# Kernel tuning notes

Measured on AMD Instinct MI355X. Metric: run time of the kernel, lower is better.

The kernel has to match this reference:

```python
import jax, jax.numpy as jnp
import numpy as np

N_NODES = 100000
N_EDGES = 800000
NUM_FEATURES = 64
HIDDEN = 16
N_GRAPHS = 64


def setup_inputs() -> dict:
    key = jax.random.key(0)
    ks = jax.random.split(key, 12)
    x = jax.random.normal(ks[0], (N_NODES, NUM_FEATURES), dtype=jnp.float32)
    edge_index = jax.random.randint(ks[1], (2, N_EDGES), 0, N_NODES, dtype=jnp.int64)
    batch = jnp.sort(jax.random.randint(ks[2], (N_NODES,), 0, N_GRAPHS, dtype=jnp.int64))
    def glorot(k, shape):
        fan_in, fan_out = shape
        s = jnp.sqrt(2.0 / (fan_in + fan_out))
        return jax.random.normal(k, shape, dtype=jnp.float32) * s
    return {
        "x": x,
        "edge_index": edge_index,
        "batch": batch,
        "W1_rel": glorot(ks[3], (NUM_FEATURES, HIDDEN)),
        "W1_root": glorot(ks[4], (NUM_FEATURES, HIDDEN)),
        "b1": jnp.zeros((HIDDEN,), dtype=jnp.float32),
        "W2_rel": glorot(ks[5], (HIDDEN, HIDDEN)),
        "W2_root": glorot(ks[6], (HIDDEN, HIDDEN)),
        "b2": jnp.zeros((HIDDEN,), dtype=jnp.float32),
        "Wlin": glorot(ks[7], (HIDDEN, 1)),
        "blin": jnp.zeros((1,), dtype=jnp.float32),
    }


def _graph_conv(h, src, dst, W_rel, W_root, b):
    # PyG GraphConv: out_i = W_rel @ sum_{j->i} h_j + b + W_root @ h_i
    agg = jax.ops.segment_sum(h[src], dst, num_segments=h.shape[0])
    return agg @ W_rel + b + h @ W_root


def reference(x, edge_index, batch, W1_rel, W1_root, b1, W2_rel, W2_root, b2, Wlin, blin):
    src, dst = edge_index[0], edge_index[1]
    h = jax.nn.relu(_graph_conv(x, src, dst, W1_rel, W1_root, b1))
    # F.dropout(training=False) is identity at inference
    h = _graph_conv(h, src, dst, W2_rel, W2_root, b2)
    # global mean pool over graphs
    sums = jax.ops.segment_sum(h, batch, num_segments=N_GRAPHS)  # [G, H]
    counts = jax.ops.segment_sum(jnp.ones((h.shape[0],), dtype=h.dtype), batch, num_segments=N_GRAPHS)
    pooled = sums / jnp.maximum(counts, 1.0)[:, None]
    out = pooled @ Wlin + blin  # [G, 1]
    return out.squeeze(1)
```

## Files before the change

### kernel.cpp

```cpp
#include <hip/hip_runtime.h>
#include <hip/hip_fp16.h>

#define BUCKET_BITS 7
#define BUCKET_N    128
#define SEG_CAP     1280
#define EPB         4096
#define EPT         16
#define OVF_CAP     16384
#define MAXBUCK     1024

__global__ __launch_bounds__(256) void k_phase1(
    const float* __restrict__ x, const float* __restrict__ Wrel,
    const float* __restrict__ Wroot, const float* __restrict__ bias,
    const int* __restrict__ src, const int* __restrict__ dst,
    __half* __restrict__ p1, float* __restrict__ r1,
    int* __restrict__ cursor, int2* __restrict__ seg,
    int* __restrict__ ovf_n, int2* __restrict__ ovf,
    int n_nodes, int n_edges, int nbuck, int tb)
{
    __shared__ int smem[2080];
    const int t = threadIdx.x;

    if ((int)blockIdx.x < tb) {
        float* s_wr = (float*)smem;
        float* s_wo = (float*)(smem + 1024);
        float* s_b  = (float*)(smem + 2048);
        for (int i = t; i < 1024; i += 256) { s_wr[i] = Wrel[i]; s_wo[i] = Wroot[i]; }
        if (t < 16) s_b[t] = bias[t];
        __syncthreads();

        const int node = blockIdx.x * 256 + t;
        if (node >= n_nodes) return;

        float accr[16], acco[16];
#pragma unroll
        for (int o = 0; o < 16; ++o) { accr[o] = 0.f; acco[o] = 0.f; }

        const float* xr = x + (size_t)node * 64;
        for (int c = 0; c < 4; ++c) {
            float4 xv[4];
#pragma unroll
            for (int u = 0; u < 4; ++u) xv[u] = *(const float4*)(xr + c * 16 + u * 4);
#pragma unroll
            for (int u = 0; u < 4; ++u) {
                const float xs[4] = {xv[u].x, xv[u].y, xv[u].z, xv[u].w};
#pragma unroll
                for (int kk = 0; kk < 4; ++kk) {
                    const int k = c * 16 + u * 4 + kk;
                    const float xk = xs[kk];
                    const float4* wr4 = (const float4*)&s_wr[k * 16];
                    const float4* wo4 = (const float4*)&s_wo[k * 16];
#pragma unroll
                    for (int q = 0; q < 4; ++q) {
                        const float4 wr = wr4[q], wo = wo4[q];
                        accr[q * 4 + 0] = fmaf(xk, wr.x, accr[q * 4 + 0]);
                        accr[q * 4 + 1] = fmaf(xk, wr.y, accr[q * 4 + 1]);
                        accr[q * 4 + 2] = fmaf(xk, wr.z, accr[q * 4 + 2]);
                        accr[q * 4 + 3] = fmaf(xk, wr.w, accr[q * 4 + 3]);
                        acco[q * 4 + 0] = fmaf(xk, wo.x, acco[q * 4 + 0]);
                        acco[q * 4 + 1] = fmaf(xk, wo.y, acco[q * 4 + 1]);
                        acco[q * 4 + 2] = fmaf(xk, wo.z, acco[q * 4 + 2]);
                        acco[q * 4 + 3] = fmaf(xk, wo.w, acco[q * 4 + 3]);
                    }
                }
            }
        }

        __half2 ph[8];
#pragma unroll
        for (int k = 0; k < 8; ++k)
            ph[k] = __floats2half2_rn(accr[2 * k], accr[2 * k + 1]);
        ((uint4*)(p1 + (size_t)node * 16))[0] = ((const uint4*)ph)[0];
        ((uint4*)(p1 + (size_t)node * 16))[1] = ((const uint4*)ph)[1];
        float* rr = r1 + (size_t)node * 16;
#pragma unroll
        for (int q = 0; q < 4; ++q) {
            float4 v;
            v.x = acco[q * 4 + 0] + s_b[q * 4 + 0];
            v.y = acco[q * 4 + 1] + s_b[q * 4 + 1];
            v.z = acco[q * 4 + 2] + s_b[q * 4 + 2];
            v.w = acco[q * 4 + 3] + s_b[q * 4 + 3];
            *(float4*)(rr + q * 4) = v;
        }
    } else {
        int* hist = smem;
        int* base = smem + 1024;
        for (int i = t; i < nbuck; i += 256) hist[i] = 0;
        __syncthreads();

        const int e0 = ((int)blockIdx.x - tb) * EPB;
        int es[EPT], ed[EPT], ep[EPT];
#pragma unroll
        for (int k = 0; k < EPT; ++k) {
            const int e = e0 + k * 256 + t;
            if (e < n_edges) {
                ed[k] = dst[e];
                es[k] = src[e];
                ep[k] = atomicAdd(&hist[ed[k] >> BUCKET_BITS], 1);
            } else ed[k] = -1;
        }
        __syncthreads();
        for (int b = t; b < nbuck; b += 256) {
            const int h = hist[b];
            base[b] = h ? atomicAdd(&cursor[b * 16], h) : 0;
        }
        __syncthreads();
#pragma unroll
        for (int k = 0; k < EPT; ++k) {
            if (ed[k] >= 0) {
                const int b = ed[k] >> BUCKET_BITS;
                const int rel = base[b] + ep[k];
                if (rel < SEG_CAP) {
                    seg[b * SEG_CAP + rel] = make_int2(es[k], ed[k]);
                } else {
                    const int op = atomicAdd(ovf_n, 1);
                    if (op < OVF_CAP) ovf[op] = make_int2(es[k], ed[k]);
                }
            }
        }
    }
}

__device__ inline void acc_half8(float* acc, uint4 raw) {
    const __half2* h2 = (const __half2*)&raw;
#pragma unroll
    for (int k = 0; k < 4; ++k) {
        const float2 f = __half22float2(h2[k]);
        acc[2 * k]     += f.x;
        acc[2 * k + 1] += f.y;
    }
}

__global__ __launch_bounds__(256) void k_aggregate(
    const __half* __restrict__ p1, const float* __restrict__ r1,
    const int2* __restrict__ seg, const int* __restrict__ cursor,
    const int* __restrict__ ovf_n, const int2* __restrict__ ovf,
    const int* __restrict__ batch,
    const float* __restrict__ W2rel, const float* __restrict__ W2root,
    const float* __restrict__ Wlin,
    float* __restrict__ s_out, float* __restrict__ T2, float* __restrict__ cntg,
    int* __restrict__ g_sorted, int* __restrict__ g_beg, int* __restrict__ g_cnt,
    int n_nodes)
{
    __shared__ int s_src[SEG_CAP];
    __shared__ int hist[BUCKET_N];
    __shared__ int iscan[BUCKET_N];
    __shared__ int cur[BUCKET_N];
    __shared__ float s_w2r[16], s_w2o[16];
    __shared__ float sT2[64], scnt[64];
    __shared__ int s_no, s_w0;

    const int t = threadIdx.x, b = blockIdx.x;
    if (t < BUCKET_N) hist[t] = 0;
    if (t < 16) {
        float ar = 0.f, ao = 0.f;
#pragma unroll
        for (int o = 0; o < 16; ++o) {
            const float wl = Wlin[o];
            ar = fmaf(W2rel[t * 16 + o], wl, ar);
            ao = fmaf(W2root[t * 16 + o], wl, ao);
        }
        s_w2r[t] = ar; s_w2o[t] = ao;
    }
    if (t < 64) { sT2[t] = 0.f; scnt[t] = 0.f; }
    if (t == 0) s_no = min(*ovf_n, OVF_CAP);
    __syncthreads();

    const int bstart = b * SEG_CAP;
    const int count = min(cursor[b * 16], SEG_CAP);

    int2 er[5];
    int ne = 0;
    for (int i = t; i < count; i += 256) {
        er[ne] = seg[bstart + i];
        atomicAdd(&hist[er[ne].y & (BUCKET_N - 1)], 1);
        ++ne;
    }
    __syncthreads();
    int v = 0;
    if (t < BUCKET_N) {
        v = hist[t];
#pragma unroll
        for (int off = 1; off < 64; off <<= 1) {
            const int u = __shfl_up(v, off);
            if ((t & 63) >= off) v += u;
        }
        if (t == 63) s_w0 = v;
    }
    __syncthreads();
    if (t < BUCKET_N) {
        if (t >= 64) v += s_w0;
        iscan[t] = v;
        cur[t] = v - hist[t];
    }
    __syncthreads();
    for (int k = 0; k < ne; ++k)
        s_src[atomicAdd(&cur[er[k].y & (BUCKET_N - 1)], 1)] = er[k].x;
    __syncthreads();

    for (int i = t; i < count; i += 256) g_sorted[bstart + i] = s_src[i];
    if (t < BUCKET_N) {
        const int nodew = b * BUCKET_N + t;
        if (nodew < n_nodes) {
            g_beg[nodew] = bstart + iscan[t] - hist[t];
            g_cnt[nodew] = hist[t];
        }
    }

    const int nl = t >> 1, half = t & 1;
    const int node = b * BUCKET_N + nl;
    if (node < n_nodes) {
        const int end = iscan[nl];
        const int beg = end - hist[nl];
        float acc[8] = {0.f, 0.f, 0.f, 0.f, 0.f, 0.f, 0.f, 0.f};
        int j = beg;
        for (; j + 2 <= end; j += 2) {
            const int s0 = s_src[j], s1 = s_src[j + 1];
            const uint4 a = *(const uint4*)(p1 + (size_t)s0 * 16 + half * 8);
            const uint4 c = *(const uint4*)(p1 + (size_t)s1 * 16 + half * 8);
            acc_half8(acc, a);
            acc_half8(acc, c);
        }
        if (j < end) {
            const uint4 a = *(const uint4*)(p1 + (size_t)s_src[j] * 16 + half * 8);
            acc_half8(acc, a);
        }
        for (int ov = 0; ov < s_no; ++ov) {
            const int2 e = ovf[ov];
            if (e.y == node) {
                const uint4 a = *(const uint4*)(p1 + (size_t)e.x * 16 + half * 8);
                acc_half8(acc, a);
            }
        }
        const float4 rA = *(const float4*)(r1 + (size_t)node * 16 + half * 8);
        const float4 rB = *(const float4*)(r1 + (size_t)node * 16 + half * 8 + 4);
        float h[8];
        h[0] = fmaxf(acc[0] + rA.x, 0.f); h[1] = fmaxf(acc[1] + rA.y, 0.f);
        h[2] = fmaxf(acc[2] + rA.z, 0.f); h[3] = fmaxf(acc[3] + rA.w, 0.f);
        h[4] = fmaxf(acc[4] + rB.x, 0.f); h[5] = fmaxf(acc[5] + rB.y, 0.f);
        h[6] = fmaxf(acc[6] + rB.z, 0.f); h[7] = fmaxf(acc[7] + rB.w, 0.f);
        float ps = 0.f, pu = 0.f;
#pragma unroll
        for (int k = 0; k < 8; ++k) {
            ps = fmaf(h[k], s_w2r[half * 8 + k], ps);
            pu = fmaf(h[k], s_w2o[half * 8 + k], pu);
        }
        ps += __shfl_xor(ps, 1);
        pu += __shfl_xor(pu, 1);
        if (half == 0) {
            s_out[node] = ps;
            const int g = batch[node];
            atomicAdd(&sT2[g], pu);
            atomicAdd(&scnt[g], 1.f);
        }
    }
    __syncthreads();
    if (t < 64) {
        if (sT2[t] != 0.f) unsafeAtomicAdd(&T2[t], sT2[t]);
        if (scnt[t] != 0.f) unsafeAtomicAdd(&cntg[t], scnt[t]);
    }
}

__global__ __launch_bounds__(256) void k_T1(
    const float* __restrict__ s_in, const int* __restrict__ g_sorted,
    const int* __restrict__ g_beg, const int* __restrict__ g_cnt,
    const int* __restrict__ batch,
    const int* __restrict__ ovf_n, const int2* __restrict__ ovf,
    float* __restrict__ T1, int n_nodes)
{
    __shared__ float bins[64];
    const int t = threadIdx.x;
    if (t < 64) bins[t] = 0.f;
    __syncthreads();

    const int node = blockIdx.x * 256 + t;
    if (node < n_nodes) {
        const int beg = g_beg[node], c = g_cnt[node];
        float acc = 0.f;
        int j = 0;
        for (; j + 4 <= c; j += 4) {
            const int a = g_sorted[beg + j],      b2 = g_sorted[beg + j + 1];
            const int cc = g_sorted[beg + j + 2], d = g_sorted[beg + j + 3];
            acc += s_in[a] + s_in[b2] + s_in[cc] + s_in[d];
        }
        for (; j < c; ++j) acc += s_in[g_sorted[beg + j]];
        if (acc != 0.f) atomicAdd(&bins[batch[node]], acc);
    }
    __syncthreads();
    if (t < 64 && bins[t] != 0.f) unsafeAtomicAdd(&T1[t], bins[t]);

    if (blockIdx.x == 0) {
        const int n = min(*ovf_n, OVF_CAP);
        for (int i = t; i < n; i += 256)
            unsafeAtomicAdd(&T1[batch[ovf[i].y]], s_in[ovf[i].x]);
    }
}

__global__ void k_finalize(
    const float* __restrict__ T1, const float* __restrict__ T2,
    const float* __restrict__ cntg, const float* __restrict__ b2,
    const float* __restrict__ Wlin, const float* __restrict__ blin,
    float* __restrict__ out, int n_graphs)
{
    const int g = threadIdx.x;
    if (g >= n_graphs) return;
    float cb = 0.f;
#pragma unroll
    for (int o = 0; o < 16; ++o) cb = fmaf(b2[o], Wlin[o], cb);
    const float c = fmaxf(cntg[g], 1.f);
    out[g] = (T1[g] + T2[g]) / c + cb + blin[0];
}

extern "C" void kernel_launch(void* const* d_in, const int* in_sizes, int n_in,
                              void* d_out, int out_size, void* d_ws, size_t ws_size,
                              hipStream_t stream) {
    const float* x       = (const float*)d_in[0];
    const int*   ei      = (const int*)d_in[1];
    const int*   batch   = (const int*)d_in[2];
    const float* W1_rel  = (const float*)d_in[3];
    const float* W1_root = (const float*)d_in[4];
    const float* b1      = (const float*)d_in[5];
    const float* W2_rel  = (const float*)d_in[6];
    const float* W2_root = (const float*)d_in[7];
    const float* b2      = (const float*)d_in[8];
    const float* Wlin    = (const float*)d_in[9];
    const float* blin    = (const float*)d_in[10];
    float* out = (float*)d_out;

    const int N = in_sizes[0] / 64;
    const int E = in_sizes[1] / 2;
    const int G = out_size;
    const int nbuck = (N + BUCKET_N - 1) >> BUCKET_BITS;

    const int* src = ei;
    const int* dst = ei + E;

    auto rnd4 = [](size_t v) { return (v + 3) & ~(size_t)3; };
    float* ws = (float*)d_ws;
    size_t off = 0;
    __half* p1      = (__half*)(ws + off); off += rnd4((size_t)N * 8);
    float* r1       = ws + off; off += rnd4((size_t)N * 16);
    float* s_buf    = ws + off; off += rnd4((size_t)N);
    int*   cursor   = (int*)(ws + off); off += rnd4((size_t)nbuck * 16);
    int*   ovf_n    = (int*)(ws + off); off += 4;
    float* T1       = ws + off; off += rnd4((size_t)G);
    float* T2       = ws + off; off += rnd4((size_t)G);
    float* cntg     = ws + off; off += rnd4((size_t)G);
    int2*  seg      = (int2*)(ws + off); off += rnd4((size_t)nbuck * SEG_CAP * 2);
    int*   g_sorted = (int*)(ws + off); off += rnd4((size_t)nbuck * SEG_CAP);
    int*   g_beg    = (int*)(ws + off); off += rnd4((size_t)N);
    int*   g_cnt    = (int*)(ws + off); off += rnd4((size_t)N);
    int2*  ovf      = (int2*)(ws + off); off += rnd4((size_t)OVF_CAP * 2);

    hipMemsetAsync(cursor, 0, ((size_t)nbuck * 16 + 4 + 3 * rnd4((size_t)G)) * sizeof(int), stream);

    const int tb = (N + 255) / 256;
    const int sb = (E + EPB - 1) / EPB;
    const int ab = (N + 255) / 256;

    k_phase1   <<<tb + sb, 256, 0, stream>>>(x, W1_rel, W1_root, b1, src, dst,
                                             p1, r1, cursor, seg, ovf_n, ovf,
                                             N, E, nbuck, tb);
    k_aggregate<<<nbuck, 256, 0, stream>>>(p1, r1, seg, cursor, ovf_n, ovf, batch,
                                           W2_rel, W2_root, Wlin, s_buf, T2, cntg,
                                           g_sorted, g_beg, g_cnt, N);
    k_T1       <<<ab, 256, 0, stream>>>(s_buf, g_sorted, g_beg, g_cnt, batch,
                                        ovf_n, ovf, T1, N);
    k_finalize <<<1, 64, 0, stream>>>(T1, T2, cntg, b2, Wlin, blin, out, G);
}
```

Baseline: 158.8 us.

## Fuse all stages into one persistent cooperative kernel with grid syncs

Replaces the four separate launches with a single cooperative persistent kernel (512 blocks, falling back to 256 or to the old multi-kernel path) that loops over work units and uses grid.sync between the transform/bin, aggregate, T1 and finalize stages. It also packs each binned edge into one int (src shifted left by 7, dst low bits) instead of an int2, halving segment-buffer traffic. The aim is to remove kernel launch gaps and inter-kernel drain. In exchange, grid-wide barriers cost time, the fixed grid may underuse the GPU for some phases, and the packing assumes node indices fit in 24 bits.

```diff
diff --git a/kernel.cpp b/kernel.cpp
--- a/kernel.cpp
+++ b/kernel.cpp
@@ -1,5 +1,8 @@
 #include <hip/hip_runtime.h>
 #include <hip/hip_fp16.h>
+#include <hip/hip_cooperative_groups.h>
+
+namespace cg = cooperative_groups;
 
 #define BUCKET_BITS 7
 #define BUCKET_N    128
@@ -7,119 +10,6 @@
 #define EPB         4096
 #define EPT         16
 #define OVF_CAP     16384
-#define MAXBUCK     1024
-
-__global__ __launch_bounds__(256) void k_phase1(
-    const float* __restrict__ x, const float* __restrict__ Wrel,
-    const float* __restrict__ Wroot, const float* __restrict__ bias,
-    const int* __restrict__ src, const int* __restrict__ dst,
-    __half* __restrict__ p1, float* __restrict__ r1,
-    int* __restrict__ cursor, int2* __restrict__ seg,
-    int* __restrict__ ovf_n, int2* __restrict__ ovf,
-    int n_nodes, int n_edges, int nbuck, int tb)
-{
-    __shared__ int smem[2080];
-    const int t = threadIdx.x;
-
-    if ((int)blockIdx.x < tb) {
-        float* s_wr = (float*)smem;
-        float* s_wo = (float*)(smem + 1024);
-        float* s_b  = (float*)(smem + 2048);
-        for (int i = t; i < 1024; i += 256) { s_wr[i] = Wrel[i]; s_wo[i] = Wroot[i]; }
-        if (t < 16) s_b[t] = bias[t];
-        __syncthreads();
-
-        const int node = blockIdx.x * 256 + t;
-        if (node >= n_nodes) return;
-
-        float accr[16], acco[16];
-#pragma unroll
-        for (int o = 0; o < 16; ++o) { accr[o] = 0.f; acco[o] = 0.f; }
-
-        const float* xr = x + (size_t)node * 64;
-        for (int c = 0; c < 4; ++c) {
-            float4 xv[4];
-#pragma unroll
-            for (int u = 0; u < 4; ++u) xv[u] = *(const float4*)(xr + c * 16 + u * 4);
-#pragma unroll
-            for (int u = 0; u < 4; ++u) {
-                const float xs[4] = {xv[u].x, xv[u].y, xv[u].z, xv[u].w};
-#pragma unroll
-                for (int kk = 0; kk < 4; ++kk) {
-                    const int k = c * 16 + u * 4 + kk;
-                    const float xk = xs[kk];
-                    const float4* wr4 = (const float4*)&s_wr[k * 16];
-                    const float4* wo4 = (const float4*)&s_wo[k * 16];
-#pragma unroll
-                    for (int q = 0; q < 4; ++q) {
-                        const float4 wr = wr4[q], wo = wo4[q];
-                        accr[q * 4 + 0] = fmaf(xk, wr.x, accr[q * 4 + 0]);
-                        accr[q * 4 + 1] = fmaf(xk, wr.y, accr[q * 4 + 1]);
-                        accr[q * 4 + 2] = fmaf(xk, wr.z, accr[q * 4 + 2]);
-                        accr[q * 4 + 3] = fmaf(xk, wr.w, accr[q * 4 + 3]);
-                        acco[q * 4 + 0] = fmaf(xk, wo.x, acco[q * 4 + 0]);
-                        acco[q * 4 + 1] = fmaf(xk, wo.y, acco[q * 4 + 1]);
-                        acco[q * 4 + 2] = fmaf(xk, wo.z, acco[q * 4 + 2]);
-                        acco[q * 4 + 3] = fmaf(xk, wo.w, acco[q * 4 + 3]);
-                    }
-                }
-            }
-        }
-
-        __half2 ph[8];
-#pragma unroll
-        for (int k = 0; k < 8; ++k)
-            ph[k] = __floats2half2_rn(accr[2 * k], accr[2 * k + 1]);
-        ((uint4*)(p1 + (size_t)node * 16))[0] = ((const uint4*)ph)[0];
-        ((uint4*)(p1 + (size_t)node * 16))[1] = ((const uint4*)ph)[1];
-        float* rr = r1 + (size_t)node * 16;
-#pragma unroll
-        for (int q = 0; q < 4; ++q) {
-            float4 v;
-            v.x = acco[q * 4 + 0] + s_b[q * 4 + 0];
-            v.y = acco[q * 4 + 1] + s_b[q * 4 + 1];
-            v.z = acco[q * 4 + 2] + s_b[q * 4 + 2];
-            v.w = acco[q * 4 + 3] + s_b[q * 4 + 3];
-            *(float4*)(rr + q * 4) = v;
-        }
-    } else {
-        int* hist = smem;
-        int* base = smem + 1024;
-        for (int i = t; i < nbuck; i += 256) hist[i] = 0;
-        __syncthreads();
-
-        const int e0 = ((int)blockIdx.x - tb) * EPB;
-        int es[EPT], ed[EPT], ep[EPT];
-#pragma unroll
-        for (int k = 0; k < EPT; ++k) {
-            const int e = e0 + k * 256 + t;
-            if (e < n_edges) {
-                ed[k] = dst[e];
-                es[k] = src[e];
-                ep[k] = atomicAdd(&hist[ed[k] >> BUCKET_BITS], 1);
-            } else ed[k] = -1;
-        }
-        __syncthreads();
-        for (int b = t; b < nbuck; b += 256) {
-            const int h = hist[b];
-            base[b] = h ? atomicAdd(&cursor[b * 16], h) : 0;
-        }
-        __syncthreads();
-#pragma unroll
-        for (int k = 0; k < EPT; ++k) {
-            if (ed[k] >= 0) {
-                const int b = ed[k] >> BUCKET_BITS;
-                const int rel = base[b] + ep[k];
-                if (rel < SEG_CAP) {
-                    seg[b * SEG_CAP + rel] = make_int2(es[k], ed[k]);
-                } else {
-                    const int op = atomicAdd(ovf_n, 1);
-                    if (op < OVF_CAP) ovf[op] = make_int2(es[k], ed[k]);
-                }
-            }
-        }
-    }
-}
 
 __device__ inline void acc_half8(float* acc, uint4 raw) {
     const __half2* h2 = (const __half2*)&raw;
@@ -131,26 +21,118 @@
     }
 }
 
-__global__ __launch_bounds__(256) void k_aggregate(
+
+__device__ __forceinline__ void transform_unit(
+    int unit, int t, int N,
+    const float* __restrict__ x, float* s_wr, float* s_wo, float* s_b,
+    __half* __restrict__ p1, float* __restrict__ r1)
+{
+    const int node = unit * 256 + t;
+    if (node >= N) return;
+    float accr[16], acco[16];
+#pragma unroll
+    for (int o = 0; o < 16; ++o) { accr[o] = 0.f; acco[o] = 0.f; }
+    const float* xr = x + (size_t)node * 64;
+    for (int c = 0; c < 4; ++c) {
+        float4 xv[4];
+#pragma unroll
+        for (int u = 0; u < 4; ++u) xv[u] = *(const float4*)(xr + c * 16 + u * 4);
+#pragma unroll
+        for (int u = 0; u < 4; ++u) {
+            const float xs[4] = {xv[u].x, xv[u].y, xv[u].z, xv[u].w};
+#pragma unroll
+            for (int kk = 0; kk < 4; ++kk) {
+                const int k = c * 16 + u * 4 + kk;
+                const float xk = xs[kk];
+                const float4* wr4 = (const float4*)&s_wr[k * 16];
+                const float4* wo4 = (const float4*)&s_wo[k * 16];
+#pragma unroll
+                for (int q = 0; q < 4; ++q) {
+                    const float4 wr = wr4[q], wo = wo4[q];
+                    accr[q * 4 + 0] = fmaf(xk, wr.x, accr[q * 4 + 0]);
+                    accr[q * 4 + 1] = fmaf(xk, wr.y, accr[q * 4 + 1]);
+                    accr[q * 4 + 2] = fmaf(xk, wr.z, accr[q * 4 + 2]);
+                    accr[q * 4 + 3] = fmaf(xk, wr.w, accr[q * 4 + 3]);
+                    acco[q * 4 + 0] = fmaf(xk, wo.x, acco[q * 4 + 0]);
+                    acco[q * 4 + 1] = fmaf(xk, wo.y, acco[q * 4 + 1]);
+                    acco[q * 4 + 2] = fmaf(xk, wo.z, acco[q * 4 + 2]);
+                    acco[q * 4 + 3] = fmaf(xk, wo.w, acco[q * 4 + 3]);
+                }
+            }
+        }
+    }
+    __half2 ph[8];
+#pragma unroll
+    for (int k = 0; k < 8; ++k)
+        ph[k] = __floats2half2_rn(accr[2 * k], accr[2 * k + 1]);
+    ((uint4*)(p1 + (size_t)node * 16))[0] = ((const uint4*)ph)[0];
+    ((uint4*)(p1 + (size_t)node * 16))[1] = ((const uint4*)ph)[1];
+    float* rr = r1 + (size_t)node * 16;
+#pragma unroll
+    for (int q = 0; q < 4; ++q) {
+        float4 v;
+        v.x = acco[q * 4 + 0] + s_b[q * 4 + 0];
+        v.y = acco[q * 4 + 1] + s_b[q * 4 + 1];
+        v.z = acco[q * 4 + 2] + s_b[q * 4 + 2];
+        v.w = acco[q * 4 + 3] + s_b[q * 4 + 3];
+        *(float4*)(rr + q * 4) = v;
+    }
+}
+
+__device__ __forceinline__ void bin_unit(
+    int unit, int t, int E, int nbuck,
+    const int* __restrict__ src, const int* __restrict__ dst,
+    int* hist, int* base,
+    int* __restrict__ cursor, int* __restrict__ seg,
+    int* __restrict__ ovf_n, int2* __restrict__ ovf)
+{
+    for (int i = t; i < nbuck; i += 256) hist[i] = 0;
+    __syncthreads();
+    const int e0 = unit * EPB;
+    int es[EPT], ed[EPT], ep[EPT];
+#pragma unroll
+    for (int k = 0; k < EPT; ++k) {
+        const int e = e0 + k * 256 + t;
+        if (e < E) {
+            ed[k] = dst[e];
+            es[k] = src[e];
+            ep[k] = atomicAdd(&hist[ed[k] >> BUCKET_BITS], 1);
+        } else ed[k] = -1;
+    }
+    __syncthreads();
+    for (int b = t; b < nbuck; b += 256) {
+        const int h = hist[b];
+        base[b] = h ? atomicAdd(&cursor[b * 16], h) : 0;
+    }
+    __syncthreads();
+#pragma unroll
+    for (int k = 0; k < EPT; ++k) {
+        if (ed[k] >= 0) {
+            const int b = ed[k] >> BUCKET_BITS;
+            const int rel = base[b] + ep[k];
+            if (rel < SEG_CAP) {
+                seg[b * SEG_CAP + rel] = (es[k] << BUCKET_BITS) | (ed[k] & (BUCKET_N - 1));
+            } else {
+                const int op = atomicAdd(ovf_n, 1);
+                if (op < OVF_CAP) ovf[op] = make_int2(es[k], ed[k]);
+            }
+        }
+    }
+}
+
+__device__ __forceinline__ void aggregate_unit(
+    int b, int t, int N,
     const __half* __restrict__ p1, const float* __restrict__ r1,
-    const int2* __restrict__ seg, const int* __restrict__ cursor,
+    const int* __restrict__ seg, const int* __restrict__ cursor,
     const int* __restrict__ ovf_n, const int2* __restrict__ ovf,
     const int* __restrict__ batch,
     const float* __restrict__ W2rel, const float* __restrict__ W2root,
     const float* __restrict__ Wlin,
-    float* __restrict__ s_out, float* __restrict__ T2, float* __restrict__ cntg,
+    float* __restrict__ s_out, float* __restrict__ T2g, float* __restrict__ cntg,
     int* __restrict__ g_sorted, int* __restrict__ g_beg, int* __restrict__ g_cnt,
-    int n_nodes)
-{
-    __shared__ int s_src[SEG_CAP];
-    __shared__ int hist[BUCKET_N];
-    __shared__ int iscan[BUCKET_N];
-    __shared__ int cur[BUCKET_N];
-    __shared__ float s_w2r[16], s_w2o[16];
-    __shared__ float sT2[64], scnt[64];
-    __shared__ int s_no, s_w0;
-
-    const int t = threadIdx.x, b = blockIdx.x;
+    int* s_src, int* hist, int* iscan, int* cur,
+    float* w2r, float* w2o, float* sT2, float* scnt, int* s_no, int* s_w0)
+{
     if (t < BUCKET_N) hist[t] = 0;
     if (t < 16) {
         float ar = 0.f, ao = 0.f;
@@ -160,20 +142,20 @@
             ar = fmaf(W2rel[t * 16 + o], wl, ar);
             ao = fmaf(W2root[t * 16 + o], wl, ao);
         }
-        s_w2r[t] = ar; s_w2o[t] = ao;
+        w2r[t] = ar; w2o[t] = ao;
     }
     if (t < 64) { sT2[t] = 0.f; scnt[t] = 0.f; }
-    if (t == 0) s_no = min(*ovf_n, OVF_CAP);
+    if (t == 0) *s_no = min(*ovf_n, OVF_CAP);
     __syncthreads();
 
     const int bstart = b * SEG_CAP;
     const int count = min(cursor[b * 16], SEG_CAP);
 
-    int2 er[5];
+    int er[5];
     int ne = 0;
     for (int i = t; i < count; i += 256) {
         er[ne] = seg[bstart + i];
-        atomicAdd(&hist[er[ne].y & (BUCKET_N - 1)], 1);
+        atomicAdd(&hist[er[ne] & (BUCKET_N - 1)], 1);
         ++ne;
     }
     __syncthreads();
@@ -185,23 +167,23 @@
             const int u = __shfl_up(v, off);
             if ((t & 63) >= off) v += u;
         }
-        if (t == 63) s_w0 = v;
+        if (t == 63) *s_w0 = v;
     }
     __syncthreads();
     if (t < BUCKET_N) {
-        if (t >= 64) v += s_w0;
+        if (t >= 64) v += *s_w0;
         iscan[t] = v;
         cur[t] = v - hist[t];
     }
     __syncthreads();
     for (int k = 0; k < ne; ++k)
-        s_src[atomicAdd(&cur[er[k].y & (BUCKET_N - 1)], 1)] = er[k].x;
+        s_src[atomicAdd(&cur[er[k] & (BUCKET_N - 1)], 1)] = er[k] >> BUCKET_BITS;
     __syncthreads();
 
     for (int i = t; i < count; i += 256) g_sorted[bstart + i] = s_src[i];
     if (t < BUCKET_N) {
         const int nodew = b * BUCKET_N + t;
-        if (nodew < n_nodes) {
+        if (nodew < N) {
             g_beg[nodew] = bstart + iscan[t] - hist[t];
             g_cnt[nodew] = hist[t];
         }
@@ -209,7 +191,7 @@
 
     const int nl = t >> 1, half = t & 1;
     const int node = b * BUCKET_N + nl;
-    if (node < n_nodes) {
+    if (node < N) {
         const int end = iscan[nl];
         const int beg = end - hist[nl];
         float acc[8] = {0.f, 0.f, 0.f, 0.f, 0.f, 0.f, 0.f, 0.f};
@@ -225,7 +207,7 @@
             const uint4 a = *(const uint4*)(p1 + (size_t)s_src[j] * 16 + half * 8);
             acc_half8(acc, a);
         }
-        for (int ov = 0; ov < s_no; ++ov) {
+        for (int ov = 0; ov < *s_no; ++ov) {
             const int2 e = ovf[ov];
             if (e.y == node) {
                 const uint4 a = *(const uint4*)(p1 + (size_t)e.x * 16 + half * 8);
@@ -242,8 +224,8 @@
         float ps = 0.f, pu = 0.f;
 #pragma unroll
         for (int k = 0; k < 8; ++k) {
-            ps = fmaf(h[k], s_w2r[half * 8 + k], ps);
-            pu = fmaf(h[k], s_w2o[half * 8 + k], pu);
+            ps = fmaf(h[k], w2r[half * 8 + k], ps);
+            pu = fmaf(h[k], w2o[half * 8 + k], pu);
         }
         ps += __shfl_xor(ps, 1);
         pu += __shfl_xor(pu, 1);
@@ -256,9 +238,164 @@
     }
     __syncthreads();
     if (t < 64) {
-        if (sT2[t] != 0.f) unsafeAtomicAdd(&T2[t], sT2[t]);
+        if (sT2[t] != 0.f) unsafeAtomicAdd(&T2g[t], sT2[t]);
         if (scnt[t] != 0.f) unsafeAtomicAdd(&cntg[t], scnt[t]);
     }
+}
+
+__device__ __forceinline__ void t1_unit(
+    int unit, int t, int N,
+    const float* __restrict__ s_in, const int* __restrict__ g_sorted,
+    const int* __restrict__ g_beg, const int* __restrict__ g_cnt,
+    const int* __restrict__ batch, float* bins, float* __restrict__ T1)
+{
+    if (t < 64) bins[t] = 0.f;
+    __syncthreads();
+    const int node = unit * 256 + t;
+    if (node < N) {
+        const int beg = g_beg[node], c = g_cnt[node];
+        float acc = 0.f;
+        int j = 0;
+        for (; j + 4 <= c; j += 4) {
+            const int a = g_sorted[beg + j],      b2i = g_sorted[beg + j + 1];
+            const int cc = g_sorted[beg + j + 2], d = g_sorted[beg + j + 3];
+            acc += s_in[a] + s_in[b2i] + s_in[cc] + s_in[d];
+        }
+        for (; j < c; ++j) acc += s_in[g_sorted[beg + j]];
+        if (acc != 0.f) atomicAdd(&bins[batch[node]], acc);
+    }
+    __syncthreads();
+    if (t < 64 && bins[t] != 0.f) unsafeAtomicAdd(&T1[t], bins[t]);
+}
+
+__global__ __launch_bounds__(256, 2) void k_mega(
+    const float* __restrict__ x, const float* __restrict__ W1rel,
+    const float* __restrict__ W1root, const float* __restrict__ b1,
+    const int* __restrict__ src, const int* __restrict__ dst,
+    const int* __restrict__ batch,
+    const float* __restrict__ W2rel, const float* __restrict__ W2root,
+    const float* __restrict__ Wlin, const float* __restrict__ b2,
+    const float* __restrict__ blin, float* __restrict__ out,
+    __half* __restrict__ p1, float* __restrict__ r1, float* __restrict__ s_buf,
+    int* __restrict__ cursor, int* __restrict__ seg,
+    int* __restrict__ ovf_n, int2* __restrict__ ovf,
+    int* __restrict__ g_sorted, int* __restrict__ g_beg, int* __restrict__ g_cnt,
+    float* __restrict__ T1, float* __restrict__ T2, float* __restrict__ cntg,
+    int N, int E, int G, int nbuck, int tb, int sb, int ab)
+{
+    cg::grid_group grid = cg::this_grid();
+    __shared__ int smem[2080];
+    const int t = threadIdx.x;
+
+    for (int wb = blockIdx.x; wb < tb + sb; wb += gridDim.x) {
+        __syncthreads();
+        if (wb < tb) {
+            float* s_wr = (float*)smem;
+            float* s_wo = (float*)smem + 1024;
+            float* s_b  = (float*)smem + 2048;
+            for (int i = t; i < 1024; i += 256) { s_wr[i] = W1rel[i]; s_wo[i] = W1root[i]; }
+            if (t < 16) s_b[t] = b1[t];
+            __syncthreads();
+            transform_unit(wb, t, N, x, s_wr, s_wo, s_b, p1, r1);
+        } else {
+            bin_unit(wb - tb, t, E, nbuck, src, dst, smem, smem + 1024,
+                     cursor, seg, ovf_n, ovf);
+        }
+    }
+    grid.sync();
+
+    {
+        int*   s_src = smem;
+        int*   hist  = smem + 1280;
+        int*   iscan = smem + 1408;
+        int*   cur   = smem + 1536;
+        float* w2r   = (float*)(smem + 1664);
+        float* w2o   = w2r + 16;
+        float* sT2   = w2o + 16;
+        float* scnt  = sT2 + 64;
+        int*   s_no  = (int*)(scnt + 64);
+        int*   s_w0  = s_no + 1;
+        for (int b = blockIdx.x; b < nbuck; b += gridDim.x) {
+            __syncthreads();
+            aggregate_unit(b, t, N, p1, r1, seg, cursor, ovf_n, ovf, batch,
+                           W2rel, W2root, Wlin, s_buf, T2, cntg,
+                           g_sorted, g_beg, g_cnt,
+                           s_src, hist, iscan, cur, w2r, w2o, sT2, scnt, s_no, s_w0);
+        }
+    }
+    grid.sync();
+
+    for (int wb = blockIdx.x; wb < ab; wb += gridDim.x) {
+        __syncthreads();
+        t1_unit(wb, t, N, s_buf, g_sorted, g_beg, g_cnt, batch, (float*)smem, T1);
+    }
+    if (blockIdx.x == 0) {
+        const int n = min(*ovf_n, OVF_CAP);
+        for (int i = t; i < n; i += 256)
+            unsafeAtomicAdd(&T1[batch[ovf[i].y]], s_buf[ovf[i].x]);
+    }
+    grid.sync();
+
+    if (blockIdx.x == 0 && t < G) {
+        float cb = 0.f;
+#pragma unroll
+        for (int o = 0; o < 16; ++o) cb = fmaf(b2[o], Wlin[o], cb);
+        const float c = fmaxf(cntg[t], 1.f);
+        out[t] = (T1[t] + T2[t]) / c + cb + blin[0];
+    }
+}
+
+__global__ __launch_bounds__(256) void k_phase1(
+    const float* __restrict__ x, const float* __restrict__ Wrel,
+    const float* __restrict__ Wroot, const float* __restrict__ bias,
+    const int* __restrict__ src, const int* __restrict__ dst,
+    __half* __restrict__ p1, float* __restrict__ r1,
+    int* __restrict__ cursor, int* __restrict__ seg,
+    int* __restrict__ ovf_n, int2* __restrict__ ovf,
+    int n_nodes, int n_edges, int nbuck, int tb)
+{
+    __shared__ int smem[2080];
+    const int t = threadIdx.x;
+    if ((int)blockIdx.x < tb) {
+        float* s_wr = (float*)smem;
+        float* s_wo = (float*)smem + 1024;
+        float* s_b  = (float*)smem + 2048;
+        for (int i = t; i < 1024; i += 256) { s_wr[i] = Wrel[i]; s_wo[i] = Wroot[i]; }
+        if (t < 16) s_b[t] = bias[t];
+        __syncthreads();
+        transform_unit(blockIdx.x, t, n_nodes, x, s_wr, s_wo, s_b, p1, r1);
+    } else {
+        bin_unit((int)blockIdx.x - tb, t, n_edges, nbuck, src, dst,
+                 smem, smem + 1024, cursor, seg, ovf_n, ovf);
+    }
+}
+
+__global__ __launch_bounds__(256) void k_aggregate(
+    const __half* __restrict__ p1, const float* __restrict__ r1,
+    const int* __restrict__ seg, const int* __restrict__ cursor,
+    const int* __restrict__ ovf_n, const int2* __restrict__ ovf,
+    const int* __restrict__ batch,
+    const float* __restrict__ W2rel, const float* __restrict__ W2root,
+    const float* __restrict__ Wlin,
+    float* __restrict__ s_out, float* __restrict__ T2, float* __restrict__ cntg,
+    int* __restrict__ g_sorted, int* __restrict__ g_beg, int* __restrict__ g_cnt,
+    int n_nodes)
+{
+    __shared__ int smem[1840];
+    int*   s_src = smem;
+    int*   hist  = smem + 1280;
+    int*   iscan = smem + 1408;
+    int*   cur   = smem + 1536;
+    float* w2r   = (float*)(smem + 1664);
+    float* w2o   = w2r + 16;
+    float* sT2   = w2o + 16;
+    float* scnt  = sT2 + 64;
+    int*   s_no  = (int*)(scnt + 64);
+    int*   s_w0  = s_no + 1;
+    aggregate_unit(blockIdx.x, threadIdx.x, n_nodes, p1, r1, seg, cursor, ovf_n, ovf,
+                   batch, W2rel, W2root, Wlin, s_out, T2, cntg,
+                   g_sorted, g_beg, g_cnt,
+                   s_src, hist, iscan, cur, w2r, w2o, sT2, scnt, s_no, s_w0);
 }
 
 __global__ __launch_bounds__(256) void k_T1(
@@ -269,29 +406,10 @@
     float* __restrict__ T1, int n_nodes)
 {
     __shared__ float bins[64];
-    const int t = threadIdx.x;
-    if (t < 64) bins[t] = 0.f;
-    __syncthreads();
-
-    const int node = blockIdx.x * 256 + t;
-    if (node < n_nodes) {
-        const int beg = g_beg[node], c = g_cnt[node];
-        float acc = 0.f;
-        int j = 0;
-        for (; j + 4 <= c; j += 4) {
-            const int a = g_sorted[beg + j],      b2 = g_sorted[beg + j + 1];
-            const int cc = g_sorted[beg + j + 2], d = g_sorted[beg + j + 3];
-            acc += s_in[a] + s_in[b2] + s_in[cc] + s_in[d];
-        }
-        for (; j < c; ++j) acc += s_in[g_sorted[beg + j]];
-        if (acc != 0.f) atomicAdd(&bins[batch[node]], acc);
-    }
-    __syncthreads();
-    if (t < 64 && bins[t] != 0.f) unsafeAtomicAdd(&T1[t], bins[t]);
-
+    t1_unit(blockIdx.x, threadIdx.x, n_nodes, s_in, g_sorted, g_beg, g_cnt, batch, bins, T1);
     if (blockIdx.x == 0) {
         const int n = min(*ovf_n, OVF_CAP);
-        for (int i = t; i < n; i += 256)
+        for (int i = threadIdx.x; i < n; i += 256)
             unsafeAtomicAdd(&T1[batch[ovf[i].y]], s_in[ovf[i].x]);
     }
 }
@@ -327,10 +445,10 @@
     const float* blin    = (const float*)d_in[10];
     float* out = (float*)d_out;
 
-    const int N = in_sizes[0] / 64;
-    const int E = in_sizes[1] / 2;
-    const int G = out_size;
-    const int nbuck = (N + BUCKET_N - 1) >> BUCKET_BITS;
+    int N = in_sizes[0] / 64;
+    int E = in_sizes[1] / 2;
+    int G = out_size;
+    int nbuck = (N + BUCKET_N - 1) >> BUCKET_BITS;
 
     const int* src = ei;
     const int* dst = ei + E;
@@ -346,7 +464,7 @@
     float* T1       = ws + off; off += rnd4((size_t)G);
     float* T2       = ws + off; off += rnd4((size_t)G);
     float* cntg     = ws + off; off += rnd4((size_t)G);
-    int2*  seg      = (int2*)(ws + off); off += rnd4((size_t)nbuck * SEG_CAP * 2);
+    int*   seg      = (int*)(ws + off); off += rnd4((size_t)nbuck * SEG_CAP);
     int*   g_sorted = (int*)(ws + off); off += rnd4((size_t)nbuck * SEG_CAP);
     int*   g_beg    = (int*)(ws + off); off += rnd4((size_t)N);
     int*   g_cnt    = (int*)(ws + off); off += rnd4((size_t)N);
@@ -354,17 +472,37 @@
 
     hipMemsetAsync(cursor, 0, ((size_t)nbuck * 16 + 4 + 3 * rnd4((size_t)G)) * sizeof(int), stream);
 
-    const int tb = (N + 255) / 256;
-    const int sb = (E + EPB - 1) / EPB;
-    const int ab = (N + 255) / 256;
-
-    k_phase1   <<<tb + sb, 256, 0, stream>>>(x, W1_rel, W1_root, b1, src, dst,
-                                             p1, r1, cursor, seg, ovf_n, ovf,
-                                             N, E, nbuck, tb);
-    k_aggregate<<<nbuck, 256, 0, stream>>>(p1, r1, seg, cursor, ovf_n, ovf, batch,
-                                           W2_rel, W2_root, Wlin, s_buf, T2, cntg,
-                                           g_sorted, g_beg, g_cnt, N);
-    k_T1       <<<ab, 256, 0, stream>>>(s_buf, g_sorted, g_beg, g_cnt, batch,
-                                        ovf_n, ovf, T1, N);
-    k_finalize <<<1, 64, 0, stream>>>(T1, T2, cntg, b2, Wlin, blin, out, G);
-}
+    int tb = (N + 255) / 256;
+    int sb = (E + EPB - 1) / EPB;
+    int ab = (N + 255) / 256;
+
+    void* args[] = {
+        (void*)&x, (void*)&W1_rel, (void*)&W1_root, (void*)&b1,
+        (void*)&src, (void*)&dst, (void*)&batch,
+        (void*)&W2_rel, (void*)&W2_root, (void*)&Wlin, (void*)&b2, (void*)&blin,
+        (void*)&out,
+        (void*)&p1, (void*)&r1, (void*)&s_buf,
+        (void*)&cursor, (void*)&seg, (void*)&ovf_n, (void*)&ovf,
+        (void*)&g_sorted, (void*)&g_beg, (void*)&g_cnt,
+        (void*)&T1, (void*)&T2, (void*)&cntg,
+        (void*)&N, (void*)&E, (void*)&G, (void*)&nbuck,
+        (void*)&tb, (void*)&sb, (void*)&ab
+    };
+
+    hipError_t err = hipLaunchCooperativeKernel((const void*)k_mega, dim3(512), dim3(256),
+                                                args, 0, stream);
+    if (err != hipSuccess)
+        err = hipLaunchCooperativeKernel((const void*)k_mega, dim3(256), dim3(256),
+                                         args, 0, stream);
+    if (err != hipSuccess) {
+        k_phase1   <<<tb + sb, 256, 0, stream>>>(x, W1_rel, W1_root, b1, src, dst,
+                                                 p1, r1, cursor, seg, ovf_n, ovf,
+                                                 N, E, nbuck, tb);
+        k_aggregate<<<nbuck, 256, 0, stream>>>(p1, r1, seg, cursor, ovf_n, ovf, batch,
+                                               W2_rel, W2_root, Wlin, s_buf, T2, cntg,
+                                               g_sorted, g_beg, g_cnt, N);
+        k_T1       <<<ab, 256, 0, stream>>>(s_buf, g_sorted, g_beg, g_cnt, batch,
+                                            ovf_n, ovf, T1, N);
+        k_finalize <<<1, 64, 0, stream>>>(T1, T2, cntg, b2, Wlin, blin, out, G);
+    }
+}
```

Result: slower. 351.3 us (+121.3%).

## Pack edge src and local dst into one int; T1 reads bucket segments directly

Applied to the files above, without the earlier changes.

Each bucketed edge is now stored as a single int holding the source index shifted left by seven bits, OR'd with the destination's low seven bits, instead of an int2 pair. This halves the segment traffic in the scatter and aggregate kernels. The aggregate kernel no longer writes the sorted source list, per-node begin and count arrays. The T1 kernel now walks each bucket's packed segment directly and maps destinations to graphs through a shared batch table. The packing limits source indices to 2^24, and T1 adds shared-memory atomics per edge.

```diff
diff --git a/kernel.cpp b/kernel.cpp
--- a/kernel.cpp
+++ b/kernel.cpp
@@ -7,14 +7,23 @@
 #define EPB         4096
 #define EPT         16
 #define OVF_CAP     16384
-#define MAXBUCK     1024
+
+__device__ inline void acc_half8(float* acc, uint4 raw) {
+    const __half2* h2 = (const __half2*)&raw;
+#pragma unroll
+    for (int k = 0; k < 4; ++k) {
+        const float2 f = __half22float2(h2[k]);
+        acc[2 * k]     += f.x;
+        acc[2 * k + 1] += f.y;
+    }
+}
 
 __global__ __launch_bounds__(256) void k_phase1(
     const float* __restrict__ x, const float* __restrict__ Wrel,
     const float* __restrict__ Wroot, const float* __restrict__ bias,
     const int* __restrict__ src, const int* __restrict__ dst,
     __half* __restrict__ p1, float* __restrict__ r1,
-    int* __restrict__ cursor, int2* __restrict__ seg,
+    int* __restrict__ cursor, int* __restrict__ seg,
     int* __restrict__ ovf_n, int2* __restrict__ ovf,
     int n_nodes, int n_edges, int nbuck, int tb)
 {
@@ -23,8 +32,8 @@
 
     if ((int)blockIdx.x < tb) {
         float* s_wr = (float*)smem;
-        float* s_wo = (float*)(smem + 1024);
-        float* s_b  = (float*)(smem + 2048);
+        float* s_wo = (float*)smem + 1024;
+        float* s_b  = (float*)smem + 2048;
         for (int i = t; i < 1024; i += 256) { s_wr[i] = Wrel[i]; s_wo[i] = Wroot[i]; }
         if (t < 16) s_b[t] = bias[t];
         __syncthreads();
@@ -35,7 +44,6 @@
         float accr[16], acco[16];
 #pragma unroll
         for (int o = 0; o < 16; ++o) { accr[o] = 0.f; acco[o] = 0.f; }
-
         const float* xr = x + (size_t)node * 64;
         for (int c = 0; c < 4; ++c) {
             float4 xv[4];
@@ -65,7 +73,6 @@
                 }
             }
         }
-
         __half2 ph[8];
 #pragma unroll
         for (int k = 0; k < 8; ++k)
@@ -111,7 +118,7 @@
                 const int b = ed[k] >> BUCKET_BITS;
                 const int rel = base[b] + ep[k];
                 if (rel < SEG_CAP) {
-                    seg[b * SEG_CAP + rel] = make_int2(es[k], ed[k]);
+                    seg[b * SEG_CAP + rel] = (es[k] << BUCKET_BITS) | (ed[k] & (BUCKET_N - 1));
                 } else {
                     const int op = atomicAdd(ovf_n, 1);
                     if (op < OVF_CAP) ovf[op] = make_int2(es[k], ed[k]);
@@ -121,25 +128,14 @@
     }
 }
 
-__device__ inline void acc_half8(float* acc, uint4 raw) {
-    const __half2* h2 = (const __half2*)&raw;
-#pragma unroll
-    for (int k = 0; k < 4; ++k) {
-        const float2 f = __half22float2(h2[k]);
-        acc[2 * k]     += f.x;
-        acc[2 * k + 1] += f.y;
-    }
-}
-
 __global__ __launch_bounds__(256) void k_aggregate(
     const __half* __restrict__ p1, const float* __restrict__ r1,
-    const int2* __restrict__ seg, const int* __restrict__ cursor,
+    const int* __restrict__ seg, const int* __restrict__ cursor,
     const int* __restrict__ ovf_n, const int2* __restrict__ ovf,
     const int* __restrict__ batch,
     const float* __restrict__ W2rel, const float* __restrict__ W2root,
     const float* __restrict__ Wlin,
     float* __restrict__ s_out, float* __restrict__ T2, float* __restrict__ cntg,
-    int* __restrict__ g_sorted, int* __restrict__ g_beg, int* __restrict__ g_cnt,
     int n_nodes)
 {
     __shared__ int s_src[SEG_CAP];
@@ -169,11 +165,11 @@
     const int bstart = b * SEG_CAP;
     const int count = min(cursor[b * 16], SEG_CAP);
 
-    int2 er[5];
+    int er[5];
     int ne = 0;
     for (int i = t; i < count; i += 256) {
         er[ne] = seg[bstart + i];
-        atomicAdd(&hist[er[ne].y & (BUCKET_N - 1)], 1);
+        atomicAdd(&hist[er[ne] & (BUCKET_N - 1)], 1);
         ++ne;
     }
     __syncthreads();
@@ -195,17 +191,8 @@
     }
     __syncthreads();
     for (int k = 0; k < ne; ++k)
-        s_src[atomicAdd(&cur[er[k].y & (BUCKET_N - 1)], 1)] = er[k].x;
-    __syncthreads();
-
-    for (int i = t; i < count; i += 256) g_sorted[bstart + i] = s_src[i];
-    if (t < BUCKET_N) {
-        const int nodew = b * BUCKET_N + t;
-        if (nodew < n_nodes) {
-            g_beg[nodew] = bstart + iscan[t] - hist[t];
-            g_cnt[nodew] = hist[t];
-        }
-    }
+        s_src[atomicAdd(&cur[er[k] & (BUCKET_N - 1)], 1)] = er[k] >> BUCKET_BITS;
+    __syncthreads();
 
     const int nl = t >> 1, half = t & 1;
     const int node = b * BUCKET_N + nl;
@@ -262,34 +249,39 @@
 }
 
 __global__ __launch_bounds__(256) void k_T1(
-    const float* __restrict__ s_in, const int* __restrict__ g_sorted,
-    const int* __restrict__ g_beg, const int* __restrict__ g_cnt,
-    const int* __restrict__ batch,
+    const float* __restrict__ s_in, const int* __restrict__ seg,
+    const int* __restrict__ cursor, const int* __restrict__ batch,
     const int* __restrict__ ovf_n, const int2* __restrict__ ovf,
     float* __restrict__ T1, int n_nodes)
 {
     __shared__ float bins[64];
-    const int t = threadIdx.x;
+    __shared__ int sbatch[BUCKET_N];
+    const int t = threadIdx.x, b = blockIdx.x;
     if (t < 64) bins[t] = 0.f;
-    __syncthreads();
-
-    const int node = blockIdx.x * 256 + t;
-    if (node < n_nodes) {
-        const int beg = g_beg[node], c = g_cnt[node];
-        float acc = 0.f;
-        int j = 0;
-        for (; j + 4 <= c; j += 4) {
-            const int a = g_sorted[beg + j],      b2 = g_sorted[beg + j + 1];
-            const int cc = g_sorted[beg + j + 2], d = g_sorted[beg + j + 3];
-            acc += s_in[a] + s_in[b2] + s_in[cc] + s_in[d];
-        }
-        for (; j < c; ++j) acc += s_in[g_sorted[beg + j]];
-        if (acc != 0.f) atomicAdd(&bins[batch[node]], acc);
+    if (t < BUCKET_N) {
+        const int node = b * BUCKET_N + t;
+        sbatch[t] = (node < n_nodes) ? batch[node] : 0;
+    }
+    __syncthreads();
+
+    const int bstart = b * SEG_CAP;
+    const int count = min(cursor[b * 16], SEG_CAP);
+    for (int i0 = t * 4; i0 < count; i0 += 1024) {
+        const int n4 = min(4, count - i0);
+        int e[4];
+#pragma unroll
+        for (int k = 0; k < 4; ++k) if (k < n4) e[k] = seg[bstart + i0 + k];
+        float vv[4];
+#pragma unroll
+        for (int k = 0; k < 4; ++k) if (k < n4) vv[k] = s_in[e[k] >> BUCKET_BITS];
+#pragma unroll
+        for (int k = 0; k < 4; ++k) if (k < n4)
+            atomicAdd(&bins[sbatch[e[k] & (BUCKET_N - 1)]], vv[k]);
     }
     __syncthreads();
     if (t < 64 && bins[t] != 0.f) unsafeAtomicAdd(&T1[t], bins[t]);
 
-    if (blockIdx.x == 0) {
+    if (b == 0) {
         const int n = min(*ovf_n, OVF_CAP);
         for (int i = t; i < n; i += 256)
             unsafeAtomicAdd(&T1[batch[ovf[i].y]], s_in[ovf[i].x]);
@@ -346,25 +338,19 @@
     float* T1       = ws + off; off += rnd4((size_t)G);
     float* T2       = ws + off; off += rnd4((size_t)G);
     float* cntg     = ws + off; off += rnd4((size_t)G);
-    int2*  seg      = (int2*)(ws + off); off += rnd4((size_t)nbuck * SEG_CAP * 2);
-    int*   g_sorted = (int*)(ws + off); off += rnd4((size_t)nbuck * SEG_CAP);
-    int*   g_beg    = (int*)(ws + off); off += rnd4((size_t)N);
-    int*   g_cnt    = (int*)(ws + off); off += rnd4((size_t)N);
+    int*   seg      = (int*)(ws + off); off += rnd4((size_t)nbuck * SEG_CAP);
     int2*  ovf      = (int2*)(ws + off); off += rnd4((size_t)OVF_CAP * 2);
 
     hipMemsetAsync(cursor, 0, ((size_t)nbuck * 16 + 4 + 3 * rnd4((size_t)G)) * sizeof(int), stream);
 
     const int tb = (N + 255) / 256;
     const int sb = (E + EPB - 1) / EPB;
-    const int ab = (N + 255) / 256;
 
     k_phase1   <<<tb + sb, 256, 0, stream>>>(x, W1_rel, W1_root, b1, src, dst,
                                              p1, r1, cursor, seg, ovf_n, ovf,
                                              N, E, nbuck, tb);
     k_aggregate<<<nbuck, 256, 0, stream>>>(p1, r1, seg, cursor, ovf_n, ovf, batch,
-                                           W2_rel, W2_root, Wlin, s_buf, T2, cntg,
-                                           g_sorted, g_beg, g_cnt, N);
-    k_T1       <<<ab, 256, 0, stream>>>(s_buf, g_sorted, g_beg, g_cnt, batch,
-                                        ovf_n, ovf, T1, N);
+                                           W2_rel, W2_root, Wlin, s_buf, T2, cntg, N);
+    k_T1       <<<nbuck, 256, 0, stream>>>(s_buf, seg, cursor, batch, ovf_n, ovf, T1, N);
     k_finalize <<<1, 64, 0, stream>>>(T1, T2, cntg, b2, Wlin, blin, out, G);
 }
```

After: 143.5 us. -9.6%, faster.
